# Kernel tuning notes

Measured on AMD Instinct MI355X. Metric: run time of the kernel, lower is better.

## Reference

```python
import jax, jax.numpy as jnp
import numpy as np

N = 100_000
E = 1_600_000
IN_FT, HID, OUT = 512, 128, 64


def setup_inputs() -> dict:
    key = jax.random.key(0)
    ks = jax.random.split(key, 7)
    x = jax.random.normal(ks[0], (N, IN_FT), dtype=jnp.float32)
    edge_index = jax.random.randint(ks[1], (2, E), 0, N, dtype=jnp.int32)
    edge_weight = jax.random.uniform(ks[2], (E,), dtype=jnp.float32)
    W1 = jax.random.normal(ks[3], (IN_FT, HID), dtype=jnp.float32) * 0.05
    b1 = jnp.zeros((HID,), dtype=jnp.float32)
    W2 = jax.random.normal(ks[4], (HID, OUT), dtype=jnp.float32) * 0.05
    b2 = jnp.zeros((OUT,), dtype=jnp.float32)
    return {"x": x, "edge_index": edge_index, "edge_weight": edge_weight,
            "W1": W1, "b1": b1, "W2": W2, "b2": b2}


def reference(x, edge_index, edge_weight, W1, b1, W2, b2):
    n = x.shape[0]
    row, col = edge_index[0], edge_index[1]
    # PyG gcn_norm: add self-loops with weight 1, symmetric normalization
    loop = jnp.arange(n, dtype=row.dtype)
    r = jnp.concatenate([row, loop])
    c = jnp.concatenate([col, loop])
    w = jnp.concatenate([edge_weight, jnp.ones((n,), edge_weight.dtype)])
    deg = jax.ops.segment_sum(w, c, num_segments=n)
    dinv = jnp.where(deg > 0, jax.lax.rsqrt(deg), 0.0)
    norm = dinv[r] * w * dinv[c]  # [E + N]

    def conv(h, W, b):
        h = h @ W                                  # [N, F_out]
        msg = norm[:, None] * h[r]                 # gather source nodes
        return jax.ops.segment_sum(msg, c, num_segments=n) + b

    h = jax.nn.relu(conv(x, W1, b1))
    # dropout: inference mode (training=False) -> identity
    out = conv(h, W2, b2)
    return jax.nn.log_softmax(out, axis=1)
```

## Files before the change

kernel.cpp:

```cpp
#include <hip/hip_runtime.h>
#include <hip/hip_fp16.h>


constexpr int NN  = 100000;
constexpr int NE  = 1600000;
constexpr int FIN = 512;
constexpr int FH  = 128;
constexpr int FO  = 64;
constexpr int CAP = 64;

constexpr int NBLK1 = 512;
constexpr int EPB   = NE / NBLK1;
constexpr int NBKT  = 196;
constexpr int BCAP  = 9728;

constexpr float WSCALE  = 32767.0f;
constexpr float IWSCALE = 1.0f / 32767.0f;

typedef _Float16 f16x8 __attribute__((ext_vector_type(8)));
typedef float    f32x4 __attribute__((ext_vector_type(4)));

union F16Frag { short4 s[2]; f16x8 v; };


__global__ __launch_bounds__(256) void k_prep(const float* __restrict__ W1,
                                              const float* __restrict__ W2,
                                              int* __restrict__ bcur,
                                              _Float16* __restrict__ w1t,
                                              _Float16* __restrict__ w2t) {
    int i = blockIdx.x * 256 + threadIdx.x;
    if (i < NBKT) bcur[i] = 0;
    if (i < FIN * FH) {
        int k = i >> 7, c = i & 127;
        w1t[c * FIN + k] = (_Float16)W1[i];
    } else if (i < FIN * FH + FH * FO) {
        int j = i - FIN * FH;
        int k = j >> 6, c = j & 63;
        w2t[c * FH + k] = (_Float16)W2[j];
    }
}


__global__ __launch_bounds__(256) void k_pass1(const int* __restrict__ rowi,
                                               const int* __restrict__ coli,
                                               const float* __restrict__ ew,
                                               int* __restrict__ bcur,
                                               unsigned long long* __restrict__ binned) {
    __shared__ unsigned long long buf[EPB];
    __shared__ int hist[NBKT];
    __shared__ int curs[NBKT];
    const int t = threadIdx.x;
    const int base = blockIdx.x * EPB;
    for (int i = t; i < NBKT; i += 256) hist[i] = 0;
    __syncthreads();
    for (int i = t; i < EPB; i += 256) {
        int e = base + i;
        int c = coli[e];
        unsigned wq = __float2uint_rn(ew[e] * WSCALE);
        buf[i] = ((unsigned long long)(unsigned)c << 32)
               | (unsigned long long)((wq << 17) | (unsigned)rowi[e]);
        atomicAdd(&hist[c >> 9], 1);
    }
    __syncthreads();
    if (t < NBKT) curs[t] = atomicAdd(&bcur[t], hist[t]);
    __syncthreads();
    for (int i = t; i < EPB; i += 256) {
        unsigned long long v = buf[i];
        int b = (int)(v >> 41);
        int pos = atomicAdd(&curs[b], 1);
        if ((unsigned)pos < BCAP) binned[(size_t)b * BCAP + pos] = v;
    }
}


__global__ __launch_bounds__(256) void k_pass2(const int* __restrict__ bcur,
                                               const unsigned long long* __restrict__ binned,
                                               unsigned* __restrict__ pay,
                                               int* __restrict__ cursor,
                                               float* __restrict__ dinv) {
    __shared__ int   cnt[512];
    __shared__ float wsum[512];
    const int t = threadIdx.x, b = blockIdx.x;
    for (int i = t; i < 512; i += 256) { cnt[i] = 0; wsum[i] = 0.f; }
    __syncthreads();
    const int total = min(bcur[b], BCAP);
    const int nbase = b * 512;
    for (int i = t; i < total; i += 256) {
        unsigned long long v = binned[(size_t)b * BCAP + i];
        int c9 = (int)((v >> 32) & 511);
        unsigned lo = (unsigned)v;
        int pos = atomicAdd(&cnt[c9], 1);
        atomicAdd(&wsum[c9], (float)(lo >> 17) * IWSCALE);
        if (pos < CAP) pay[(size_t)(nbase + c9) * CAP + pos] = lo;
    }
    __syncthreads();
    for (int i = t; i < 512; i += 256) {
        int node = nbase + i;
        if (node < NN) {
            cursor[node] = cnt[i];
            dinv[node]   = rsqrtf(1.0f + wsum[i]);
        }
    }
}


__global__ __launch_bounds__(256) void k_gemm1(const float* __restrict__ X,
                                               const _Float16* __restrict__ w1t,
                                               _Float16* __restrict__ H1) {
    __shared__ __align__(16) _Float16 As[64 * 64];
    __shared__ __align__(16) _Float16 Bs[128 * 64];
    const int tid  = threadIdx.x;
    const int brow = blockIdx.x * 64;
    const int wid = tid >> 6, l = tid & 63;
    const int wr = wid >> 1, wc = wid & 1;
    const int l15 = l & 15, lg = l >> 4;

    f32x4 acc[2][4];
#pragma unroll
    for (int m = 0; m < 2; ++m)
#pragma unroll
        for (int n = 0; n < 4; ++n) acc[m][n] = (f32x4){0.f, 0.f, 0.f, 0.f};

    const int ar    = tid >> 2;
    const int apart = tid & 3;
    const int grow  = brow + ar;
    const int br    = tid >> 1;
    const int bhalf = tid & 1;

    for (int k0 = 0; k0 < FIN; k0 += 64) {
#pragma unroll
        for (int h = 0; h < 2; ++h) {
            int slot = apart * 2 + h;
            float4 lo = make_float4(0.f, 0.f, 0.f, 0.f), hi = lo;
            if (grow < NN) {
                lo = *(const float4*)&X[(size_t)grow * FIN + k0 + slot * 8];
                hi = *(const float4*)&X[(size_t)grow * FIN + k0 + slot * 8 + 4];
            }
            union { _Float16 f[8]; int4 v; } pk;
            pk.f[0] = (_Float16)lo.x; pk.f[1] = (_Float16)lo.y;
            pk.f[2] = (_Float16)lo.z; pk.f[3] = (_Float16)lo.w;
            pk.f[4] = (_Float16)hi.x; pk.f[5] = (_Float16)hi.y;
            pk.f[6] = (_Float16)hi.z; pk.f[7] = (_Float16)hi.w;
            *(int4*)&As[ar * 64 + ((slot ^ (ar & 7)) * 8)] = pk.v;
        }
#pragma unroll
        for (int j = 0; j < 4; ++j) {
            int slot = bhalf * 4 + j;
            *(int4*)&Bs[br * 64 + ((slot ^ (br & 7)) * 8)] =
                *(const int4*)&w1t[br * FIN + k0 + slot * 8];
        }
        __syncthreads();
#pragma unroll
        for (int ks = 0; ks < 2; ++ks) {
            F16Frag au[2], bu[4];
            int klo = ks * 32 + 4 * lg;
            int khi = klo + 16;
#pragma unroll
            for (int m = 0; m < 2; ++m) {
                int row = wr * 32 + m * 16 + l15;
                int sw  = row & 7;
                au[m].s[0] = *(const short4*)&As[row * 64 + (((klo >> 3) ^ sw) * 8) + (klo & 7)];
                au[m].s[1] = *(const short4*)&As[row * 64 + (((khi >> 3) ^ sw) * 8) + (khi & 7)];
            }
#pragma unroll
            for (int n = 0; n < 4; ++n) {
                int row = wc * 64 + n * 16 + l15;
                int sw  = row & 7;
                bu[n].s[0] = *(const short4*)&Bs[row * 64 + (((klo >> 3) ^ sw) * 8) + (klo & 7)];
                bu[n].s[1] = *(const short4*)&Bs[row * 64 + (((khi >> 3) ^ sw) * 8) + (khi & 7)];
            }
#pragma unroll
            for (int m = 0; m < 2; ++m)
#pragma unroll
                for (int n = 0; n < 4; ++n)
                    acc[m][n] = __builtin_amdgcn_mfma_f32_16x16x32_f16(
                        au[m].v, bu[n].v, acc[m][n], 0, 0, 0);
        }
        __syncthreads();
    }
#pragma unroll
    for (int m = 0; m < 2; ++m)
#pragma unroll
        for (int n = 0; n < 4; ++n) {
            int gcol = wc * 64 + n * 16 + l15;
#pragma unroll
            for (int r = 0; r < 4; ++r) {
                int gr = brow + wr * 32 + m * 16 + lg * 4 + r;
                if (gr < NN) H1[(size_t)gr * FH + gcol] = (_Float16)acc[m][n][r];
            }
        }
}


__global__ __launch_bounds__(256) void k_gemm2(const _Float16* __restrict__ H2,
                                               const _Float16* __restrict__ w2t,
                                               _Float16* __restrict__ H3) {
    __shared__ __align__(16) _Float16 As[64 * 128];
    __shared__ __align__(16) _Float16 Bs[64 * 128];
    const int tid  = threadIdx.x;
    const int brow = blockIdx.x * 64;
    const int wid = tid >> 6, l = tid & 63;
    const int wr = wid >> 1, wc = wid & 1;
    const int l15 = l & 15, lg = l >> 4;

    f32x4 acc[2][2];
#pragma unroll
    for (int m = 0; m < 2; ++m)
#pragma unroll
        for (int n = 0; n < 2; ++n) acc[m][n] = (f32x4){0.f, 0.f, 0.f, 0.f};

    {
        int ar = tid >> 2, part = tid & 3, grow = brow + ar;
#pragma unroll
        for (int j = 0; j < 4; ++j) {
            int slot = part * 4 + j;
            int4 v = make_int4(0, 0, 0, 0);
            if (grow < NN) v = *(const int4*)&H2[(size_t)grow * FH + slot * 8];
            *(int4*)&As[ar * 128 + ((slot ^ (ar & 15)) * 8)] = v;
            *(int4*)&Bs[ar * 128 + ((slot ^ (ar & 15)) * 8)] =
                *(const int4*)&w2t[ar * FH + slot * 8];
        }
    }
    __syncthreads();
#pragma unroll
    for (int ks = 0; ks < 4; ++ks) {
        F16Frag au[2], bu[2];
        int klo = ks * 32 + 4 * lg;
        int khi = klo + 16;
#pragma unroll
        for (int m = 0; m < 2; ++m) {
            int row = wr * 32 + m * 16 + l15;
            int sw  = row & 15;
            au[m].s[0] = *(const short4*)&As[row * 128 + (((klo >> 3) ^ sw) * 8) + (klo & 7)];
            au[m].s[1] = *(const short4*)&As[row * 128 + (((khi >> 3) ^ sw) * 8) + (khi & 7)];
        }
#pragma unroll
        for (int n = 0; n < 2; ++n) {
            int row = wc * 32 + n * 16 + l15;
            int sw  = row & 15;
            bu[n].s[0] = *(const short4*)&Bs[row * 128 + (((klo >> 3) ^ sw) * 8) + (klo & 7)];
            bu[n].s[1] = *(const short4*)&Bs[row * 128 + (((khi >> 3) ^ sw) * 8) + (khi & 7)];
        }
#pragma unroll
        for (int m = 0; m < 2; ++m)
#pragma unroll
            for (int n = 0; n < 2; ++n)
                acc[m][n] = __builtin_amdgcn_mfma_f32_16x16x32_f16(
                    au[m].v, bu[n].v, acc[m][n], 0, 0, 0);
    }
#pragma unroll
    for (int m = 0; m < 2; ++m)
#pragma unroll
        for (int n = 0; n < 2; ++n) {
            int gcol = wc * 32 + n * 16 + l15;
#pragma unroll
            for (int r = 0; r < 4; ++r) {
                int gr = brow + wr * 32 + m * 16 + lg * 4 + r;
                if (gr < NN) H3[(size_t)gr * FO + gcol] = (_Float16)acc[m][n][r];
            }
        }
}


__global__ __launch_bounds__(256) void k_agg1(const int* __restrict__ cursor,
                                              const unsigned* __restrict__ pay,
                                              const float* __restrict__ dinv,
                                              const __half* __restrict__ H1,
                                              const float* __restrict__ b1,
                                              __half* __restrict__ H2) {
    int node = (blockIdx.x * 256 + threadIdx.x) >> 6;
    int lane = threadIdx.x & 63;
    if (node >= NN) return;
    const int f = lane * 2;
    float dc = dinv[node];
    float2 hc = __half22float2(*(const __half2*)&H1[(size_t)node * FH + f]);
    float a0x = dc * dc * hc.x, a0y = dc * dc * hc.y;
    float a1x = 0, a1y = 0, a2x = 0, a2y = 0, a3x = 0, a3y = 0;
    int cnt = min(max(cursor[node], 0), CAP);
    const unsigned* p = &pay[(size_t)node * CAP];
    int e = 0;
    for (; e + 4 <= cnt; e += 4) {
        unsigned v0 = p[e], v1 = p[e + 1], v2 = p[e + 2], v3 = p[e + 3];
        int s0 = v0 & 0x1FFFF, s1 = v1 & 0x1FFFF;
        int s2 = v2 & 0x1FFFF, s3 = v3 & 0x1FFFF;
        float w0 = (float)(v0 >> 17) * IWSCALE * dinv[s0] * dc;
        float w1 = (float)(v1 >> 17) * IWSCALE * dinv[s1] * dc;
        float w2 = (float)(v2 >> 17) * IWSCALE * dinv[s2] * dc;
        float w3 = (float)(v3 >> 17) * IWSCALE * dinv[s3] * dc;
        float2 g0 = __half22float2(*(const __half2*)&H1[(size_t)s0 * FH + f]);
        float2 g1 = __half22float2(*(const __half2*)&H1[(size_t)s1 * FH + f]);
        float2 g2 = __half22float2(*(const __half2*)&H1[(size_t)s2 * FH + f]);
        float2 g3 = __half22float2(*(const __half2*)&H1[(size_t)s3 * FH + f]);
        a0x += w0 * g0.x; a0y += w0 * g0.y;
        a1x += w1 * g1.x; a1y += w1 * g1.y;
        a2x += w2 * g2.x; a2y += w2 * g2.y;
        a3x += w3 * g3.x; a3y += w3 * g3.y;
    }
    for (; e < cnt; ++e) {
        unsigned v = p[e];
        int s = v & 0x1FFFF;
        float w = (float)(v >> 17) * IWSCALE * dinv[s] * dc;
        float2 g = __half22float2(*(const __half2*)&H1[(size_t)s * FH + f]);
        a0x += w * g.x; a0y += w * g.y;
    }
    float vx = a0x + a1x + a2x + a3x + b1[f];
    float vy = a0y + a1y + a2y + a3y + b1[f + 1];
    vx = vx > 0.f ? vx : 0.f;
    vy = vy > 0.f ? vy : 0.f;
    *(__half2*)&H2[(size_t)node * FH + f] = __floats2half2_rn(vx, vy);
}


__global__ __launch_bounds__(256) void k_agg2(const int* __restrict__ cursor,
                                              const unsigned* __restrict__ pay,
                                              const float* __restrict__ dinv,
                                              const __half* __restrict__ H3,
                                              const float* __restrict__ b2,
                                              float* __restrict__ out) {
    int node = (blockIdx.x * 256 + threadIdx.x) >> 6;
    int lane = threadIdx.x & 63;
    if (node >= NN) return;
    float dc = dinv[node];
    float a0 = dc * dc * __half2float(H3[(size_t)node * FO + lane]);
    float a1 = 0, a2 = 0, a3 = 0;
    int cnt = min(max(cursor[node], 0), CAP);
    const unsigned* p = &pay[(size_t)node * CAP];
    int e = 0;
    for (; e + 4 <= cnt; e += 4) {
        unsigned v0 = p[e], v1 = p[e + 1], v2 = p[e + 2], v3 = p[e + 3];
        int s0 = v0 & 0x1FFFF, s1 = v1 & 0x1FFFF;
        int s2 = v2 & 0x1FFFF, s3 = v3 & 0x1FFFF;
        float w0 = (float)(v0 >> 17) * IWSCALE * dinv[s0] * dc;
        float w1 = (float)(v1 >> 17) * IWSCALE * dinv[s1] * dc;
        float w2 = (float)(v2 >> 17) * IWSCALE * dinv[s2] * dc;
        float w3 = (float)(v3 >> 17) * IWSCALE * dinv[s3] * dc;
        a0 += w0 * __half2float(H3[(size_t)s0 * FO + lane]);
        a1 += w1 * __half2float(H3[(size_t)s1 * FO + lane]);
        a2 += w2 * __half2float(H3[(size_t)s2 * FO + lane]);
        a3 += w3 * __half2float(H3[(size_t)s3 * FO + lane]);
    }
    for (; e < cnt; ++e) {
        unsigned v = p[e];
        int s = v & 0x1FFFF;
        float w = (float)(v >> 17) * IWSCALE * dinv[s] * dc;
        a0 += w * __half2float(H3[(size_t)s * FO + lane]);
    }
    float v = a0 + a1 + a2 + a3 + b2[lane];
    float m = v;
#pragma unroll
    for (int s = 32; s; s >>= 1) m = fmaxf(m, __shfl_xor(m, s));
    float ex = expf(v - m);
    float sum = ex;
#pragma unroll
    for (int s = 32; s; s >>= 1) sum += __shfl_xor(sum, s);
    out[(size_t)node * FO + lane] = v - m - logf(sum);
}


extern "C" void kernel_launch(void* const* d_in, const int* in_sizes, int n_in,
                              void* d_out, int out_size, void* d_ws, size_t ws_size,
                              hipStream_t stream) {
    const float* x   = (const float*)d_in[0];
    const int*   ei  = (const int*)d_in[1];
    const int*   row = ei;
    const int*   col = ei + NE;
    const float* ew  = (const float*)d_in[2];
    const float* W1  = (const float*)d_in[3];
    const float* b1  = (const float*)d_in[4];
    const float* W2  = (const float*)d_in[5];
    const float* b2  = (const float*)d_in[6];
    float* out = (float*)d_out;

    int*       bcur   = (int*)d_ws;
    int*       cursor = bcur + 256;
    float*     dinv   = (float*)(cursor + 102400);
    _Float16*  w1t    = (_Float16*)(dinv + 102400);
    _Float16*  w2t    = w1t + FIN * FH;
    unsigned long long* binned = (unsigned long long*)(w2t + FH * FO);
    unsigned*  pay    = (unsigned*)(binned + (size_t)NBKT * BCAP);
    _Float16*  H1     = (_Float16*)(pay + (size_t)NN * CAP);
    _Float16*  H2     = H1 + (size_t)NN * FH;
    _Float16*  H3     = H2 + (size_t)NN * FH;

    k_prep <<<(FIN * FH + FH * FO + 255) / 256, 256, 0, stream>>>(W1, W2, bcur, w1t, w2t);
    k_pass1<<<NBLK1, 256, 0, stream>>>(row, col, ew, bcur, binned);
    k_pass2<<<NBKT, 256, 0, stream>>>(bcur, binned, pay, cursor, dinv);

    k_gemm1<<<(NN + 63) / 64, 256, 0, stream>>>(x, w1t, H1);
    k_agg1 <<<(NN * 64 + 255) / 256, 256, 0, stream>>>(cursor, pay, dinv,
                                                       (const __half*)H1, b1, (__half*)H2);
    k_gemm2<<<(NN + 63) / 64, 256, 0, stream>>>(H2, w2t, H3);
    k_agg2 <<<(NN * 64 + 255) / 256, 256, 0, stream>>>(cursor, pay, dinv,
                                                       (const __half*)H3, b2, out);
}
```

Measured before the change: 278.7 us.

## Fold weight prep into pass1, remap gemm1 blocks per XCD, unroll aggregation by eight

The weight transpose and fp16 conversion move from a separate k_prep kernel into k_pass1, and the bucket-counter reset becomes a hipMemsetAsync. This removes one kernel launch. gemm1 remaps block IDs so that consecutive row tiles land on the same XCD. Both aggregation kernels now read payload entries with two uint4 vector loads and unroll the gather loop by eight, and the constant scale is folded into one per-node multiplier. The point is to keep more gathers in flight and to cut the number of instructions per edge, at the cost of higher register pressure.

```diff
diff --git a/kernel.cpp b/kernel.cpp
--- a/kernel.cpp
+++ b/kernel.cpp
@@ -13,6 +13,7 @@
 constexpr int EPB   = NE / NBLK1;
 constexpr int NBKT  = 196;
 constexpr int BCAP  = 9728;
+constexpr int NWT   = FIN * FH + FH * FO;
 
 constexpr float WSCALE  = 32767.0f;
 constexpr float IWSCALE = 1.0f / 32767.0f;
@@ -21,35 +22,32 @@
 typedef float    f32x4 __attribute__((ext_vector_type(4)));
 
 union F16Frag { short4 s[2]; f16x8 v; };
-
-
-__global__ __launch_bounds__(256) void k_prep(const float* __restrict__ W1,
-                                              const float* __restrict__ W2,
-                                              int* __restrict__ bcur,
-                                              _Float16* __restrict__ w1t,
-                                              _Float16* __restrict__ w2t) {
-    int i = blockIdx.x * 256 + threadIdx.x;
-    if (i < NBKT) bcur[i] = 0;
-    if (i < FIN * FH) {
-        int k = i >> 7, c = i & 127;
-        w1t[c * FIN + k] = (_Float16)W1[i];
-    } else if (i < FIN * FH + FH * FO) {
-        int j = i - FIN * FH;
-        int k = j >> 6, c = j & 63;
-        w2t[c * FH + k] = (_Float16)W2[j];
-    }
-}
 
 
 __global__ __launch_bounds__(256) void k_pass1(const int* __restrict__ rowi,
                                                const int* __restrict__ coli,
                                                const float* __restrict__ ew,
+                                               const float* __restrict__ W1,
+                                               const float* __restrict__ W2,
+                                               _Float16* __restrict__ w1t,
+                                               _Float16* __restrict__ w2t,
                                                int* __restrict__ bcur,
                                                unsigned long long* __restrict__ binned) {
     __shared__ unsigned long long buf[EPB];
     __shared__ int hist[NBKT];
     __shared__ int curs[NBKT];
     const int t = threadIdx.x;
+    {
+        int i = blockIdx.x * 256 + t;
+        if (i < FIN * FH) {
+            int k = i >> 7, c = i & 127;
+            w1t[c * FIN + k] = (_Float16)W1[i];
+        } else if (i < NWT) {
+            int j = i - FIN * FH;
+            int k = j >> 6, c = j & 63;
+            w2t[c * FH + k] = (_Float16)W2[j];
+        }
+    }
     const int base = blockIdx.x * EPB;
     for (int i = t; i < NBKT; i += 256) hist[i] = 0;
     __syncthreads();
@@ -110,7 +108,11 @@
     __shared__ __align__(16) _Float16 As[64 * 64];
     __shared__ __align__(16) _Float16 Bs[128 * 64];
     const int tid  = threadIdx.x;
-    const int brow = blockIdx.x * 64;
+    const int nwg = gridDim.x;
+    const int q = nwg >> 3, r = nwg & 7;
+    const int xcd = blockIdx.x & 7, idx = blockIdx.x >> 3;
+    const int wg = (xcd < r ? xcd * (q + 1) : r * (q + 1) + (xcd - r) * q) + idx;
+    const int brow = wg * 64;
     const int wid = tid >> 6, l = tid & 63;
     const int wr = wid >> 1, wc = wid & 1;
     const int l15 = l & 15, lg = l >> 4;
@@ -184,9 +186,9 @@
         for (int n = 0; n < 4; ++n) {
             int gcol = wc * 64 + n * 16 + l15;
 #pragma unroll
-            for (int r = 0; r < 4; ++r) {
-                int gr = brow + wr * 32 + m * 16 + lg * 4 + r;
-                if (gr < NN) H1[(size_t)gr * FH + gcol] = (_Float16)acc[m][n][r];
+            for (int r4 = 0; r4 < 4; ++r4) {
+                int gr = brow + wr * 32 + m * 16 + lg * 4 + r4;
+                if (gr < NN) H1[(size_t)gr * FH + gcol] = (_Float16)acc[m][n][r4];
             }
         }
 }
@@ -254,9 +256,9 @@
         for (int n = 0; n < 2; ++n) {
             int gcol = wc * 32 + n * 16 + l15;
 #pragma unroll
-            for (int r = 0; r < 4; ++r) {
-                int gr = brow + wr * 32 + m * 16 + lg * 4 + r;
-                if (gr < NN) H3[(size_t)gr * FO + gcol] = (_Float16)acc[m][n][r];
+            for (int r4 = 0; r4 < 4; ++r4) {
+                int gr = brow + wr * 32 + m * 16 + lg * 4 + r4;
+                if (gr < NN) H3[(size_t)gr * FO + gcol] = (_Float16)acc[m][n][r4];
             }
         }
 }
@@ -272,34 +274,44 @@
     int lane = threadIdx.x & 63;
     if (node >= NN) return;
     const int f = lane * 2;
-    float dc = dinv[node];
+    float dc  = dinv[node];
+    float dcs = dc * IWSCALE;
     float2 hc = __half22float2(*(const __half2*)&H1[(size_t)node * FH + f]);
     float a0x = dc * dc * hc.x, a0y = dc * dc * hc.y;
     float a1x = 0, a1y = 0, a2x = 0, a2y = 0, a3x = 0, a3y = 0;
     int cnt = min(max(cursor[node], 0), CAP);
     const unsigned* p = &pay[(size_t)node * CAP];
     int e = 0;
-    for (; e + 4 <= cnt; e += 4) {
-        unsigned v0 = p[e], v1 = p[e + 1], v2 = p[e + 2], v3 = p[e + 3];
-        int s0 = v0 & 0x1FFFF, s1 = v1 & 0x1FFFF;
-        int s2 = v2 & 0x1FFFF, s3 = v3 & 0x1FFFF;
-        float w0 = (float)(v0 >> 17) * IWSCALE * dinv[s0] * dc;
-        float w1 = (float)(v1 >> 17) * IWSCALE * dinv[s1] * dc;
-        float w2 = (float)(v2 >> 17) * IWSCALE * dinv[s2] * dc;
-        float w3 = (float)(v3 >> 17) * IWSCALE * dinv[s3] * dc;
+    for (; e + 8 <= cnt; e += 8) {
+        uint4 pa = *(const uint4*)&p[e];
+        uint4 pb = *(const uint4*)&p[e + 4];
+        int s0 = pa.x & 0x1FFFF, s1 = pa.y & 0x1FFFF, s2 = pa.z & 0x1FFFF, s3 = pa.w & 0x1FFFF;
+        int s4 = pb.x & 0x1FFFF, s5 = pb.y & 0x1FFFF, s6 = pb.z & 0x1FFFF, s7 = pb.w & 0x1FFFF;
+        float w0 = (float)(pa.x >> 17) * dcs * dinv[s0];
+        float w1 = (float)(pa.y >> 17) * dcs * dinv[s1];
+        float w2 = (float)(pa.z >> 17) * dcs * dinv[s2];
+        float w3 = (float)(pa.w >> 17) * dcs * dinv[s3];
+        float w4 = (float)(pb.x >> 17) * dcs * dinv[s4];
+        float w5 = (float)(pb.y >> 17) * dcs * dinv[s5];
+        float w6 = (float)(pb.z >> 17) * dcs * dinv[s6];
+        float w7 = (float)(pb.w >> 17) * dcs * dinv[s7];
         float2 g0 = __half22float2(*(const __half2*)&H1[(size_t)s0 * FH + f]);
         float2 g1 = __half22float2(*(const __half2*)&H1[(size_t)s1 * FH + f]);
         float2 g2 = __half22float2(*(const __half2*)&H1[(size_t)s2 * FH + f]);
         float2 g3 = __half22float2(*(const __half2*)&H1[(size_t)s3 * FH + f]);
-        a0x += w0 * g0.x; a0y += w0 * g0.y;
-        a1x += w1 * g1.x; a1y += w1 * g1.y;
-        a2x += w2 * g2.x; a2y += w2 * g2.y;
-        a3x += w3 * g3.x; a3y += w3 * g3.y;
+        float2 g4 = __half22float2(*(const __half2*)&H1[(size_t)s4 * FH + f]);
+        float2 g5 = __half22float2(*(const __half2*)&H1[(size_t)s5 * FH + f]);
+        float2 g6 = __half22float2(*(const __half2*)&H1[(size_t)s6 * FH + f]);
+        float2 g7 = __half22float2(*(const __half2*)&H1[(size_t)s7 * FH + f]);
+        a0x += w0 * g0.x; a0y += w0 * g0.y;  a1x += w1 * g1.x; a1y += w1 * g1.y;
+        a2x += w2 * g2.x; a2y += w2 * g2.y;  a3x += w3 * g3.x; a3y += w3 * g3.y;
+        a0x += w4 * g4.x; a0y += w4 * g4.y;  a1x += w5 * g5.x; a1y += w5 * g5.y;
+        a2x += w6 * g6.x; a2y += w6 * g6.y;  a3x += w7 * g7.x; a3y += w7 * g7.y;
     }
     for (; e < cnt; ++e) {
         unsigned v = p[e];
         int s = v & 0x1FFFF;
-        float w = (float)(v >> 17) * IWSCALE * dinv[s] * dc;
+        float w = (float)(v >> 17) * dcs * dinv[s];
         float2 g = __half22float2(*(const __half2*)&H1[(size_t)s * FH + f]);
         a0x += w * g.x; a0y += w * g.y;
     }
@@ -320,29 +332,39 @@
     int node = (blockIdx.x * 256 + threadIdx.x) >> 6;
     int lane = threadIdx.x & 63;
     if (node >= NN) return;
-    float dc = dinv[node];
+    float dc  = dinv[node];
+    float dcs = dc * IWSCALE;
     float a0 = dc * dc * __half2float(H3[(size_t)node * FO + lane]);
     float a1 = 0, a2 = 0, a3 = 0;
     int cnt = min(max(cursor[node], 0), CAP);
     const unsigned* p = &pay[(size_t)node * CAP];
     int e = 0;
-    for (; e + 4 <= cnt; e += 4) {
-        unsigned v0 = p[e], v1 = p[e + 1], v2 = p[e + 2], v3 = p[e + 3];
-        int s0 = v0 & 0x1FFFF, s1 = v1 & 0x1FFFF;
-        int s2 = v2 & 0x1FFFF, s3 = v3 & 0x1FFFF;
-        float w0 = (float)(v0 >> 17) * IWSCALE * dinv[s0] * dc;
-        float w1 = (float)(v1 >> 17) * IWSCALE * dinv[s1] * dc;
-        float w2 = (float)(v2 >> 17) * IWSCALE * dinv[s2] * dc;
-        float w3 = (float)(v3 >> 17) * IWSCALE * dinv[s3] * dc;
+    for (; e + 8 <= cnt; e += 8) {
+        uint4 pa = *(const uint4*)&p[e];
+        uint4 pb = *(const uint4*)&p[e + 4];
+        int s0 = pa.x & 0x1FFFF, s1 = pa.y & 0x1FFFF, s2 = pa.z & 0x1FFFF, s3 = pa.w & 0x1FFFF;
+        int s4 = pb.x & 0x1FFFF, s5 = pb.y & 0x1FFFF, s6 = pb.z & 0x1FFFF, s7 = pb.w & 0x1FFFF;
+        float w0 = (float)(pa.x >> 17) * dcs * dinv[s0];
+        float w1 = (float)(pa.y >> 17) * dcs * dinv[s1];
+        float w2 = (float)(pa.z >> 17) * dcs * dinv[s2];
+        float w3 = (float)(pa.w >> 17) * dcs * dinv[s3];
+        float w4 = (float)(pb.x >> 17) * dcs * dinv[s4];
+        float w5 = (float)(pb.y >> 17) * dcs * dinv[s5];
+        float w6 = (float)(pb.z >> 17) * dcs * dinv[s6];
+        float w7 = (float)(pb.w >> 17) * dcs * dinv[s7];
         a0 += w0 * __half2float(H3[(size_t)s0 * FO + lane]);
         a1 += w1 * __half2float(H3[(size_t)s1 * FO + lane]);
         a2 += w2 * __half2float(H3[(size_t)s2 * FO + lane]);
         a3 += w3 * __half2float(H3[(size_t)s3 * FO + lane]);
+        a0 += w4 * __half2float(H3[(size_t)s4 * FO + lane]);
+        a1 += w5 * __half2float(H3[(size_t)s5 * FO + lane]);
+        a2 += w6 * __half2float(H3[(size_t)s6 * FO + lane]);
+        a3 += w7 * __half2float(H3[(size_t)s7 * FO + lane]);
     }
     for (; e < cnt; ++e) {
         unsigned v = p[e];
         int s = v & 0x1FFFF;
-        float w = (float)(v >> 17) * IWSCALE * dinv[s] * dc;
+        float w = (float)(v >> 17) * dcs * dinv[s];
         a0 += w * __half2float(H3[(size_t)s * FO + lane]);
     }
     float v = a0 + a1 + a2 + a3 + b2[lane];
@@ -382,8 +404,8 @@
     _Float16*  H2     = H1 + (size_t)NN * FH;
     _Float16*  H3     = H2 + (size_t)NN * FH;
 
-    k_prep <<<(FIN * FH + FH * FO + 255) / 256, 256, 0, stream>>>(W1, W2, bcur, w1t, w2t);
-    k_pass1<<<NBLK1, 256, 0, stream>>>(row, col, ew, bcur, binned);
+    hipMemsetAsync(bcur, 0, NBKT * sizeof(int), stream);
+    k_pass1<<<NBLK1, 256, 0, stream>>>(row, col, ew, W1, W2, w1t, w2t, bcur, binned);
     k_pass2<<<NBKT, 256, 0, stream>>>(bcur, binned, pay, cursor, dinv);
 
     k_gemm1<<<(NN + 63) / 64, 256, 0, stream>>>(x, w1t, H1);
```

Measured after the change: 282.4 us. About the same (+1.3%).
